# Kernel tuning notes

Hardware: AMD Instinct MI355X
Metric: run time of the kernel (lower is better)

## Reference

```python
import jax, jax.numpy as jnp
import numpy as np

R, S, C, HID = 8192, 128, 32, 64   # rays, samples/ray, grid_chn, mlp_hidden_chn
G = 128                            # voxel grid resolution
COLOR_CHN = 3
NUM_HARM = 3
OPACITY_INIT_BIAS = -5.0
GAIN = 1.0
HE_DIM = 3 * 2 * NUM_HARM + 3      # harmonic embedding dim = 21

def _relu(x):
    return jnp.maximum(x, 0.0)

def _trilinear(grid, p):
    # grid: [G, G, G, Cg] indexed [z, y, x]; p: [N, 3] xyz coords in [-1, 1]
    g = grid.shape[0]
    c = (p + 1.0) * 0.5 * (g - 1)  # align_corners=True convention
    c0f = jnp.floor(c)
    fr = c - c0f
    c0 = jnp.clip(c0f.astype(jnp.int32), 0, g - 1)
    c1 = jnp.clip(c0 + 1, 0, g - 1)
    x0, y0, z0 = c0[:, 0], c0[:, 1], c0[:, 2]
    x1, y1, z1 = c1[:, 0], c1[:, 1], c1[:, 2]
    fx, fy, fz = fr[:, 0:1], fr[:, 1:2], fr[:, 2:3]
    out = jnp.zeros((p.shape[0], grid.shape[-1]), grid.dtype)
    for xi, wx in ((x0, 1.0 - fx), (x1, fx)):
        for yi, wy in ((y0, 1.0 - fy), (y1, fy)):
            for zi, wz in ((z0, 1.0 - fz), (z1, fz)):
                out = out + (wx * wy * wz) * grid[zi, yi, xi]
    return out

def _harmonic(d):
    # [sin(2^i d), cos(2^i d)] for i<NUM_HARM, with raw direction appended
    freqs = 2.0 ** jnp.arange(NUM_HARM, dtype=jnp.float32)
    ang = d[:, None, :] * freqs[None, :, None]  # [R, NH, 3]
    n = d.shape[0]
    return jnp.concatenate([jnp.sin(ang).reshape(n, -1), jnp.cos(ang).reshape(n, -1), d], axis=-1)

def _forward(origins, directions, near, far, feature_grid, Wr, br, Wt1, bt1, Wt2, bt2, Wo1, bo1, Wo2, bo2, Wc1, bc1, Wc2, bc2):
    n_rays = origins.shape[0]
    # stratified midpoints between near and far
    t = near[:, None] + (far - near)[:, None] * (jnp.arange(S, dtype=jnp.float32) + 0.5) / S
    pts = origins[:, None, :] + t[..., None] * directions[:, None, :]  # [R, S, 3]
    feats = _trilinear(feature_grid, pts.reshape(-1, 3)).reshape(n_rays, S, -1)
    # trunk MLP
    e = _relu(feats @ Wt1 + bt1)
    e = _relu(e @ Wt2 + bt2)
    # opacity MLP (last-layer bias carries opacity_init_bias)
    raw = _relu(e @ Wo1 + bo1) @ Wo2 + bo2  # [R, S, 1]
    density = jax.nn.softplus(GAIN * raw[..., 0])
    delta = ((far - near) / S)[:, None]
    alpha = 1.0 - jnp.exp(-delta * density)  # [R, S]
    trans = jnp.cumprod(1.0 - alpha, axis=1)
    T = jnp.concatenate([jnp.ones((n_rays, 1), alpha.dtype), trans[:, :-1]], axis=1)
    w = T * alpha  # compositing weights
    # color branch: harmonic ray-direction encoding added to color-MLP input
    ray_enc = _harmonic(directions) @ Wr + br  # [R, HID]
    cin = e + ray_enc[:, None, :]
    col = jax.nn.sigmoid(_relu(cin @ Wc1 + bc1) @ Wc2 + bc2)  # [R, S, COLOR_CHN]
    color = jnp.einsum('rs,rsc->rc', w, col)
    mask = 1.0 - trans[:, -1]
    color = color + (1.0 - mask)[:, None] * 0.0  # bg_color = 0.0
    return color, mask

def setup_inputs():
    key = jax.random.key(0)
    ks = jax.random.split(key, 16)
    directions = jax.random.normal(ks[0], (R, 3), jnp.float32)
    directions = directions / jnp.linalg.norm(directions, axis=-1, keepdims=True)
    origins = jnp.zeros((R, 3), jnp.float32)
    near = jnp.full((R,), 0.1, jnp.float32)
    far = jnp.full((R,), 1.0, jnp.float32)
    feature_grid = jax.random.normal(ks[1], (G, G, G, C), jnp.float32) * 0.1
    def lin(k, i, o):
        s = (2.0 / (i + o)) ** 0.5
        return jax.random.normal(k, (i, o), jnp.float32) * s
    return {
        'origins': origins, 'directions': directions, 'near': near, 'far': far,
        'feature_grid': feature_grid,
        'Wr': lin(ks[2], HE_DIM, HID), 'br': jnp.zeros((HID,), jnp.float32),
        'Wt1': lin(ks[3], C, HID), 'bt1': jnp.zeros((HID,), jnp.float32),
        'Wt2': lin(ks[4], HID, HID), 'bt2': jnp.zeros((HID,), jnp.float32),
        'Wo1': lin(ks[5], HID, HID), 'bo1': jnp.zeros((HID,), jnp.float32),
        'Wo2': lin(ks[6], HID, 1), 'bo2': jnp.full((1,), OPACITY_INIT_BIAS, jnp.float32),
        'Wc1': lin(ks[7], HID, HID), 'bc1': jnp.zeros((HID,), jnp.float32),
        'Wc2': lin(ks[8], HID, COLOR_CHN), 'bc2': jnp.zeros((COLOR_CHN,), jnp.float32),
    }

def reference(origins, directions, near, far, feature_grid, Wr, br, Wt1, bt1, Wt2, bt2, Wo1, bo1, Wo2, bo2, Wc1, bc1, Wc2, bc2):
    return _forward(origins, directions, near, far, feature_grid, Wr, br, Wt1, bt1, Wt2, bt2, Wo1, bo1, Wo2, bo2, Wc1, bc1, Wc2, bc2)
```

## Files before the change

### kernel.cpp

```cpp
#include <hip/hip_runtime.h>
#include <hip/hip_bf16.h>
#include <math.h>

#define NRAYS 8192

typedef short s16x8 __attribute__((ext_vector_type(8)));
typedef float f32x4 __attribute__((ext_vector_type(4)));

__device__ __forceinline__ unsigned pk2(float a, float b){
  union { __hip_bfloat162 h; unsigned u; } cv;
  cv.h = __float22bfloat162_rn(make_float2(a, b));
  return cv.u;
}
__device__ __forceinline__ unsigned short f2bf(float x){
  unsigned u = __float_as_uint(x);
  u += 0x7FFF + ((u >> 16) & 1);
  return (unsigned short)(u >> 16);
}
__device__ __forceinline__ float softplusf_(float x){ return (x > 20.f) ? x : log1pf(expf(x)); }
__device__ __forceinline__ float sigmoidf_(float x){ return 1.f / (1.f + expf(-x)); }

__global__ void prep_weights(const float* __restrict__ Wt1, const float* __restrict__ Wt2,
                             const float* __restrict__ Wo1, const float* __restrict__ Wc1,
                             unsigned short* __restrict__ ws)
{
  const int i0 = blockIdx.x * blockDim.x + threadIdx.x;
  const int st = gridDim.x * blockDim.x;
  for (int i = i0; i < 2048; i += st){ int n = i >> 5, k = i & 31; ws[i]         = f2bf(Wt1[k * 64 + n]); }
  for (int i = i0; i < 4096; i += st){ int n = i >> 6, k = i & 63; ws[2048 + i]  = f2bf(Wt2[k * 64 + n]); }
  for (int i = i0; i < 4096; i += st){ int n = i >> 6, k = i & 63; ws[6144 + i]  = f2bf(Wo1[k * 64 + n]); }
  for (int i = i0; i < 4096; i += st){ int n = i >> 6, k = i & 63; ws[10240 + i] = f2bf(Wc1[k * 64 + n]); }
}

extern "C" __global__ __launch_bounds__(256, 4)
void lightplane_fwd(const float* __restrict__ origins, const float* __restrict__ dirs,
                    const float* __restrict__ nearv,   const float* __restrict__ farv,
                    const float* __restrict__ grid,
                    const float* __restrict__ Wr,  const float* __restrict__ br,
                    const float* __restrict__ bt1, const float* __restrict__ bt2,
                    const float* __restrict__ bo1,
                    const float* __restrict__ Wo2, const float* __restrict__ bo2,
                    const float* __restrict__ bc1,
                    const float* __restrict__ Wc2, const float* __restrict__ bc2,
                    const unsigned short* __restrict__ ws,
                    float* __restrict__ out)
{
  __shared__ float s_scr[4 * 2304];
  __shared__ float s_enc[2][64];
  __shared__ float s_wtot[2][2];
  __shared__ float s_part[2][2][3];

  const int tid  = threadIdx.x;
  const int lane = tid & 63, wv = tid >> 6;
  const int ln15 = lane & 15, quad = lane >> 4;
  const int r_loc = wv >> 1, hh = wv & 1;
  const int ray  = blockIdx.x * 2 + r_loc;
  const int s_idx = hh * 64 + lane;

  float*          wbase = s_scr + wv * 2304;
  unsigned*       uscr  = (unsigned*)wbase;
  unsigned short* fscr  = (unsigned short*)wbase;

  if (tid < 128) {
    const int rr = tid >> 6, j = tid & 63;
    const int rg = blockIdx.x * 2 + rr;
    const float ddx = dirs[rg * 3 + 0], ddy = dirs[rg * 3 + 1], ddz = dirs[rg * 3 + 2];
    float h[21]; float f = 1.f;
#pragma unroll
    for (int q = 0; q < 3; ++q) {
      h[q * 3 + 0] = sinf(ddx * f); h[q * 3 + 1] = sinf(ddy * f); h[q * 3 + 2] = sinf(ddz * f);
      h[9 + q * 3 + 0] = cosf(ddx * f); h[9 + q * 3 + 1] = cosf(ddy * f); h[9 + q * 3 + 2] = cosf(ddz * f);
      f *= 2.f;
    }
    h[18] = ddx; h[19] = ddy; h[20] = ddz;
    float a = br[j];
#pragma unroll
    for (int i = 0; i < 21; ++i) a = fmaf(h[i], Wr[i * 64 + j], a);
    s_enc[rr][j] = a;
  }

  const float dx = dirs[ray * 3 + 0], dy = dirs[ray * 3 + 1], dz = dirs[ray * 3 + 2];
  const float ox = origins[ray * 3 + 0], oy = origins[ray * 3 + 1], oz = origins[ray * 3 + 2];
  const float nr = nearv[ray], fa = farv[ray];
  const float t  = nr + (fa - nr) * ((s_idx + 0.5f) * (1.0f / 128.0f));
  const float px = fmaf(t, dx, ox), py = fmaf(t, dy, oy), pz = fmaf(t, dz, oz);

  const float cx = (px + 1.f) * 63.5f, cy = (py + 1.f) * 63.5f, cz = (pz + 1.f) * 63.5f;
  const float fx0 = floorf(cx), fy0 = floorf(cy), fz0 = floorf(cz);
  const float frx = cx - fx0, fry = cy - fy0, frz = cz - fz0;
  int ix0 = min(max((int)fx0, 0), 127), iy0 = min(max((int)fy0, 0), 127), iz0 = min(max((int)fz0, 0), 127);
  int ix1 = min(ix0 + 1, 127), iy1 = min(iy0 + 1, 127), iz1 = min(iz0 + 1, 127);
  const float wxs[2] = {1.f - frx, frx}, wys[2] = {1.f - fry, fry}, wzs[2] = {1.f - frz, frz};
  const int xi[2] = {ix0, ix1}, yi[2] = {iy0, iy1}, zi[2] = {iz0, iz1};

  float fe[32];
#pragma unroll
  for (int k = 0; k < 32; ++k) fe[k] = 0.f;
#pragma unroll
  for (int a = 0; a < 2; ++a)
#pragma unroll
    for (int b2i = 0; b2i < 2; ++b2i)
#pragma unroll
      for (int c2 = 0; c2 < 2; ++c2) {
        const float wgt = wzs[a] * wys[b2i] * wxs[c2];
        const float4* g4 = (const float4*)(grid + ((size_t)((zi[a] * 128 + yi[b2i]) * 128 + xi[c2])) * 32);
#pragma unroll
        for (int k = 0; k < 8; ++k) {
          float4 g = g4[k];
          fe[4 * k + 0] = fmaf(wgt, g.x, fe[4 * k + 0]);
          fe[4 * k + 1] = fmaf(wgt, g.y, fe[4 * k + 1]);
          fe[4 * k + 2] = fmaf(wgt, g.z, fe[4 * k + 2]);
          fe[4 * k + 3] = fmaf(wgt, g.w, fe[4 * k + 3]);
        }
      }

  {
    unsigned* frow = uscr + lane * 20;
#pragma unroll
    for (int q = 0; q < 4; ++q) {
      uint4 v;
      v.x = pk2(fe[8 * q + 0], fe[8 * q + 1]); v.y = pk2(fe[8 * q + 2], fe[8 * q + 3]);
      v.z = pk2(fe[8 * q + 4], fe[8 * q + 5]); v.w = pk2(fe[8 * q + 6], fe[8 * q + 7]);
      *(uint4*)(frow + 4 * q) = v;
    }
  }
  __syncthreads();

  s16x8 b1[4];
#pragma unroll
  for (int nt = 0; nt < 4; ++nt)
    b1[nt] = *(const s16x8*)(fscr + (16 * nt + ln15) * 40 + quad * 8);

#pragma unroll
  for (int mt = 0; mt < 4; ++mt) {
    s16x8 a1 = *(const s16x8*)(ws + (16 * mt + ln15) * 32 + quad * 8);
    float4 bb = *(const float4*)(bt1 + 16 * mt + 4 * quad);
    f32x4 acc[4];
#pragma unroll
    for (int nt = 0; nt < 4; ++nt) {
      f32x4 c; c[0] = bb.x; c[1] = bb.y; c[2] = bb.z; c[3] = bb.w;
      acc[nt] = __builtin_amdgcn_mfma_f32_16x16x32_bf16(a1, b1[nt], c, 0, 0, 0);
    }
#pragma unroll
    for (int nt = 0; nt < 4; ++nt) {
      uint2 p;
      p.x = pk2(fmaxf(acc[nt][0], 0.f), fmaxf(acc[nt][1], 0.f));
      p.y = pk2(fmaxf(acc[nt][2], 0.f), fmaxf(acc[nt][3], 0.f));
      *(uint2*)(uscr + (16 * nt + ln15) * 36 + 8 * mt + 2 * quad) = p;
    }
  }
  s16x8 b2[4][2];
#pragma unroll
  for (int nt = 0; nt < 4; ++nt)
#pragma unroll
    for (int ks = 0; ks < 2; ++ks)
      b2[nt][ks] = *(const s16x8*)(uscr + (16 * nt + ln15) * 36 + 16 * ks + 4 * quad);

#pragma unroll
  for (int mt = 0; mt < 4; ++mt) {
    float4 bb = *(const float4*)(bt2 + 16 * mt + 4 * quad);
    f32x4 acc[4];
#pragma unroll
    for (int nt = 0; nt < 4; ++nt) { f32x4 c; c[0]=bb.x;c[1]=bb.y;c[2]=bb.z;c[3]=bb.w; acc[nt]=c; }
#pragma unroll
    for (int ks = 0; ks < 2; ++ks) {
      s16x8 a = *(const s16x8*)(ws + 2048 + (16 * mt + ln15) * 64 + ks * 32 + quad * 8);
#pragma unroll
      for (int nt = 0; nt < 4; ++nt)
        acc[nt] = __builtin_amdgcn_mfma_f32_16x16x32_bf16(a, b2[nt][ks], acc[nt], 0, 0, 0);
    }
    float4 en = *(const float4*)(&s_enc[r_loc][16 * mt + 4 * quad]);
#pragma unroll
    for (int nt = 0; nt < 4; ++nt) {
      uint2 p;
      p.x = pk2(fmaxf(acc[nt][0], 0.f) + en.x, fmaxf(acc[nt][1], 0.f) + en.y);
      p.y = pk2(fmaxf(acc[nt][2], 0.f) + en.z, fmaxf(acc[nt][3], 0.f) + en.w);
      *(uint2*)(uscr + (16 * nt + ln15) * 36 + 8 * mt + 2 * quad) = p;
    }
  }
  s16x8 b4[4][2];
#pragma unroll
  for (int nt = 0; nt < 4; ++nt)
#pragma unroll
    for (int ks = 0; ks < 2; ++ks)
      b4[nt][ks] = *(const s16x8*)(uscr + (16 * nt + ln15) * 36 + 16 * ks + 4 * quad);

#pragma unroll
  for (int mt = 0; mt < 4; ++mt) {
    float4 bb = *(const float4*)(bt2 + 16 * mt + 4 * quad);
    f32x4 acc[4];
#pragma unroll
    for (int nt = 0; nt < 4; ++nt) { f32x4 c; c[0]=bb.x;c[1]=bb.y;c[2]=bb.z;c[3]=bb.w; acc[nt]=c; }
#pragma unroll
    for (int ks = 0; ks < 2; ++ks) {
      s16x8 a = *(const s16x8*)(ws + 2048 + (16 * mt + ln15) * 64 + ks * 32 + quad * 8);
#pragma unroll
      for (int nt = 0; nt < 4; ++nt)
        acc[nt] = __builtin_amdgcn_mfma_f32_16x16x32_bf16(a, b2[nt][ks], acc[nt], 0, 0, 0);
    }
#pragma unroll
    for (int nt = 0; nt < 4; ++nt) {
      uint2 p;
      p.x = pk2(fmaxf(acc[nt][0], 0.f), fmaxf(acc[nt][1], 0.f));
      p.y = pk2(fmaxf(acc[nt][2], 0.f), fmaxf(acc[nt][3], 0.f));
      *(uint2*)(uscr + (16 * nt + ln15) * 36 + 8 * mt + 2 * quad) = p;
    }
  }
  s16x8 b3[4][2];
#pragma unroll
  for (int nt = 0; nt < 4; ++nt)
#pragma unroll
    for (int ks = 0; ks < 2; ++ks)
      b3[nt][ks] = *(const s16x8*)(uscr + (16 * nt + ln15) * 36 + 16 * ks + 4 * quad);

  float p_o[4] = {0.f, 0.f, 0.f, 0.f};
  float pc0[4] = {0.f, 0.f, 0.f, 0.f}, pc1[4] = {0.f, 0.f, 0.f, 0.f}, pc2[4] = {0.f, 0.f, 0.f, 0.f};
#pragma unroll
  for (int mt = 0; mt < 4; ++mt) {
    {
      float4 bb = *(const float4*)(bo1 + 16 * mt + 4 * quad);
      f32x4 acc[4];
#pragma unroll
      for (int nt = 0; nt < 4; ++nt) { f32x4 c; c[0]=bb.x;c[1]=bb.y;c[2]=bb.z;c[3]=bb.w; acc[nt]=c; }
#pragma unroll
      for (int ks = 0; ks < 2; ++ks) {
        s16x8 a = *(const s16x8*)(ws + 6144 + (16 * mt + ln15) * 64 + ks * 32 + quad * 8);
#pragma unroll
        for (int nt = 0; nt < 4; ++nt)
          acc[nt] = __builtin_amdgcn_mfma_f32_16x16x32_bf16(a, b3[nt][ks], acc[nt], 0, 0, 0);
      }
      float4 wo = *(const float4*)(Wo2 + 16 * mt + 4 * quad);
#pragma unroll
      for (int nt = 0; nt < 4; ++nt)
        p_o[nt] += fmaxf(acc[nt][0], 0.f) * wo.x + fmaxf(acc[nt][1], 0.f) * wo.y +
                   fmaxf(acc[nt][2], 0.f) * wo.z + fmaxf(acc[nt][3], 0.f) * wo.w;
    }
    {
      float4 bb = *(const float4*)(bc1 + 16 * mt + 4 * quad);
      f32x4 acc[4];
#pragma unroll
      for (int nt = 0; nt < 4; ++nt) { f32x4 c; c[0]=bb.x;c[1]=bb.y;c[2]=bb.z;c[3]=bb.w; acc[nt]=c; }
#pragma unroll
      for (int ks = 0; ks < 2; ++ks) {
        s16x8 a = *(const s16x8*)(ws + 10240 + (16 * mt + ln15) * 64 + ks * 32 + quad * 8);
#pragma unroll
        for (int nt = 0; nt < 4; ++nt)
          acc[nt] = __builtin_amdgcn_mfma_f32_16x16x32_bf16(a, b4[nt][ks], acc[nt], 0, 0, 0);
      }
      float wcf[12];
      const float* wc = Wc2 + (16 * mt + 4 * quad) * 3;
      *(float4*)&wcf[0] = ((const float4*)wc)[0];
      *(float4*)&wcf[4] = ((const float4*)wc)[1];
      *(float4*)&wcf[8] = ((const float4*)wc)[2];
#pragma unroll
      for (int nt = 0; nt < 4; ++nt)
#pragma unroll
        for (int r = 0; r < 4; ++r) {
          const float hv = fmaxf(acc[nt][r], 0.f);
          pc0[nt] = fmaf(hv, wcf[r * 3 + 0], pc0[nt]);
          pc1[nt] = fmaf(hv, wcf[r * 3 + 1], pc1[nt]);
          pc2[nt] = fmaf(hv, wcf[r * 3 + 2], pc2[nt]);
        }
    }
  }
#pragma unroll
  for (int nt = 0; nt < 4; ++nt) {
    p_o[nt] += __shfl_xor(p_o[nt], 16, 64); p_o[nt] += __shfl_xor(p_o[nt], 32, 64);
    pc0[nt] += __shfl_xor(pc0[nt], 16, 64); pc0[nt] += __shfl_xor(pc0[nt], 32, 64);
    pc1[nt] += __shfl_xor(pc1[nt], 16, 64); pc1[nt] += __shfl_xor(pc1[nt], 32, 64);
    pc2[nt] += __shfl_xor(pc2[nt], 16, 64); pc2[nt] += __shfl_xor(pc2[nt], 32, 64);
  }

  const float delta = (fa - nr) * (1.0f / 128.0f);
  const float bo2v = bo2[0], bc2x = bc2[0], bc2y = bc2[1], bc2z = bc2[2];
  float A_[4], C0[4], C1[4], C2[4];
#pragma unroll
  for (int nt = 0; nt < 4; ++nt) {
    const float dens = softplusf_(p_o[nt] + bo2v);
    A_[nt] = 1.f - expf(-delta * dens);
    C0[nt] = sigmoidf_(pc0[nt] + bc2x);
    C1[nt] = sigmoidf_(pc1[nt] + bc2y);
    C2[nt] = sigmoidf_(pc2[nt] + bc2z);
  }
  const float a_own = (quad < 2) ? (quad == 0 ? A_[0] : A_[1]) : (quad == 2 ? A_[2] : A_[3]);
  const float c0own = (quad < 2) ? (quad == 0 ? C0[0] : C0[1]) : (quad == 2 ? C0[2] : C0[3]);
  const float c1own = (quad < 2) ? (quad == 0 ? C1[0] : C1[1]) : (quad == 2 ? C1[2] : C1[3]);
  const float c2own = (quad < 2) ? (quad == 0 ? C2[0] : C2[1]) : (quad == 2 ? C2[2] : C2[3]);

  float v = 1.f - a_own;
#pragma unroll
  for (int off = 1; off < 64; off <<= 1) {
    const float u = __shfl_up(v, off, 64);
    if (lane >= off) v *= u;
  }
  const float tot = __shfl(v, 63, 64);
  if (lane == 0) s_wtot[r_loc][hh] = tot;
  float excl = __shfl_up(v, 1, 64);
  if (lane == 0) excl = 1.f;
  __syncthreads();
  const float prefix = hh ? s_wtot[r_loc][0] : 1.f;
  const float Ttot   = s_wtot[r_loc][0] * s_wtot[r_loc][1];
  const float wgt = prefix * excl * a_own;

  float p0 = wgt * c0own, p1 = wgt * c1own, p2 = wgt * c2own;
#pragma unroll
  for (int off = 32; off > 0; off >>= 1) {
    p0 += __shfl_down(p0, off, 64);
    p1 += __shfl_down(p1, off, 64);
    p2 += __shfl_down(p2, off, 64);
  }
  if (lane == 0) { s_part[r_loc][hh][0] = p0; s_part[r_loc][hh][1] = p1; s_part[r_loc][hh][2] = p2; }
  __syncthreads();
  if (hh == 0 && lane == 0) {
    out[ray * 3 + 0] = s_part[r_loc][0][0] + s_part[r_loc][1][0];
    out[ray * 3 + 1] = s_part[r_loc][0][1] + s_part[r_loc][1][1];
    out[ray * 3 + 2] = s_part[r_loc][0][2] + s_part[r_loc][1][2];
    out[NRAYS * 3 + ray] = 1.f - Ttot;
  }
}

extern "C" void kernel_launch(void* const* d_in, const int* in_sizes, int n_in,
                              void* d_out, int out_size, void* d_ws, size_t ws_size,
                              hipStream_t stream)
{
  (void)in_sizes; (void)n_in; (void)out_size; (void)ws_size;
  const float* origins = (const float*)d_in[0];
  const float* dirs    = (const float*)d_in[1];
  const float* nearv   = (const float*)d_in[2];
  const float* farv    = (const float*)d_in[3];
  const float* grid    = (const float*)d_in[4];
  const float* Wr  = (const float*)d_in[5];
  const float* br  = (const float*)d_in[6];
  const float* Wt1 = (const float*)d_in[7];
  const float* bt1 = (const float*)d_in[8];
  const float* Wt2 = (const float*)d_in[9];
  const float* bt2 = (const float*)d_in[10];
  const float* Wo1 = (const float*)d_in[11];
  const float* bo1 = (const float*)d_in[12];
  const float* Wo2 = (const float*)d_in[13];
  const float* bo2 = (const float*)d_in[14];
  const float* Wc1 = (const float*)d_in[15];
  const float* bc1 = (const float*)d_in[16];
  const float* Wc2 = (const float*)d_in[17];
  const float* bc2 = (const float*)d_in[18];
  unsigned short* ws = (unsigned short*)d_ws;
  float* out = (float*)d_out;

  prep_weights<<<16, 256, 0, stream>>>(Wt1, Wt2, Wo1, Wc1, ws);
  lightplane_fwd<<<NRAYS / 2, 256, 0, stream>>>(origins, dirs, nearv, farv, grid,
                                                Wr, br, bt1, bt2, bo1, Wo2, bo2,
                                                bc1, Wc2, bc2, ws, out);
}
```

Measured before the change: 591.4 us.

## Compute trunk layer-2 GEMM once and add ray encoding in registers

The old code ran the second trunk GEMM twice: once with the ray encoding added for the color branch and once without it for the opacity branch. Now it runs once and feeds the result to the opacity MLP. It then adds the per-ray encoding to the bf16 B fragments in registers before the color GEMM, removing one GEMM and one LDS round trip. The extra bf16 rounding (bf16 value plus encoding, rounded again) differs slightly from rounding the fp32 sum. The launch-bounds occupancy hint is also lowered from 4 to 3 blocks per CU.

```diff
diff --git a/kernel.cpp b/kernel.cpp
--- a/kernel.cpp
+++ b/kernel.cpp
@@ -17,6 +17,7 @@
   u += 0x7FFF + ((u >> 16) & 1);
   return (unsigned short)(u >> 16);
 }
+__device__ __forceinline__ float bf2f(unsigned short s){ return __uint_as_float(((unsigned)s) << 16); }
 __device__ __forceinline__ float softplusf_(float x){ return (x > 20.f) ? x : log1pf(expf(x)); }
 __device__ __forceinline__ float sigmoidf_(float x){ return 1.f / (1.f + expf(-x)); }
 
@@ -32,7 +33,7 @@
   for (int i = i0; i < 4096; i += st){ int n = i >> 6, k = i & 63; ws[10240 + i] = f2bf(Wc1[k * 64 + n]); }
 }
 
-extern "C" __global__ __launch_bounds__(256, 4)
+extern "C" __global__ __launch_bounds__(256, 3)
 void lightplane_fwd(const float* __restrict__ origins, const float* __restrict__ dirs,
                     const float* __restrict__ nearv,   const float* __restrict__ farv,
                     const float* __restrict__ grid,
@@ -169,35 +170,6 @@
       for (int nt = 0; nt < 4; ++nt)
         acc[nt] = __builtin_amdgcn_mfma_f32_16x16x32_bf16(a, b2[nt][ks], acc[nt], 0, 0, 0);
     }
-    float4 en = *(const float4*)(&s_enc[r_loc][16 * mt + 4 * quad]);
-#pragma unroll
-    for (int nt = 0; nt < 4; ++nt) {
-      uint2 p;
-      p.x = pk2(fmaxf(acc[nt][0], 0.f) + en.x, fmaxf(acc[nt][1], 0.f) + en.y);
-      p.y = pk2(fmaxf(acc[nt][2], 0.f) + en.z, fmaxf(acc[nt][3], 0.f) + en.w);
-      *(uint2*)(uscr + (16 * nt + ln15) * 36 + 8 * mt + 2 * quad) = p;
-    }
-  }
-  s16x8 b4[4][2];
-#pragma unroll
-  for (int nt = 0; nt < 4; ++nt)
-#pragma unroll
-    for (int ks = 0; ks < 2; ++ks)
-      b4[nt][ks] = *(const s16x8*)(uscr + (16 * nt + ln15) * 36 + 16 * ks + 4 * quad);
-
-#pragma unroll
-  for (int mt = 0; mt < 4; ++mt) {
-    float4 bb = *(const float4*)(bt2 + 16 * mt + 4 * quad);
-    f32x4 acc[4];
-#pragma unroll
-    for (int nt = 0; nt < 4; ++nt) { f32x4 c; c[0]=bb.x;c[1]=bb.y;c[2]=bb.z;c[3]=bb.w; acc[nt]=c; }
-#pragma unroll
-    for (int ks = 0; ks < 2; ++ks) {
-      s16x8 a = *(const s16x8*)(ws + 2048 + (16 * mt + ln15) * 64 + ks * 32 + quad * 8);
-#pragma unroll
-      for (int nt = 0; nt < 4; ++nt)
-        acc[nt] = __builtin_amdgcn_mfma_f32_16x16x32_bf16(a, b2[nt][ks], acc[nt], 0, 0, 0);
-    }
 #pragma unroll
     for (int nt = 0; nt < 4; ++nt) {
       uint2 p;
@@ -214,55 +186,73 @@
       b3[nt][ks] = *(const s16x8*)(uscr + (16 * nt + ln15) * 36 + 16 * ks + 4 * quad);
 
   float p_o[4] = {0.f, 0.f, 0.f, 0.f};
+#pragma unroll
+  for (int mt = 0; mt < 4; ++mt) {
+    float4 bb = *(const float4*)(bo1 + 16 * mt + 4 * quad);
+    f32x4 acc[4];
+#pragma unroll
+    for (int nt = 0; nt < 4; ++nt) { f32x4 c; c[0]=bb.x;c[1]=bb.y;c[2]=bb.z;c[3]=bb.w; acc[nt]=c; }
+#pragma unroll
+    for (int ks = 0; ks < 2; ++ks) {
+      s16x8 a = *(const s16x8*)(ws + 6144 + (16 * mt + ln15) * 64 + ks * 32 + quad * 8);
+#pragma unroll
+      for (int nt = 0; nt < 4; ++nt)
+        acc[nt] = __builtin_amdgcn_mfma_f32_16x16x32_bf16(a, b3[nt][ks], acc[nt], 0, 0, 0);
+    }
+    float4 wo = *(const float4*)(Wo2 + 16 * mt + 4 * quad);
+#pragma unroll
+    for (int nt = 0; nt < 4; ++nt)
+      p_o[nt] += fmaxf(acc[nt][0], 0.f) * wo.x + fmaxf(acc[nt][1], 0.f) * wo.y +
+                 fmaxf(acc[nt][2], 0.f) * wo.z + fmaxf(acc[nt][3], 0.f) * wo.w;
+  }
+
+#pragma unroll
+  for (int ks = 0; ks < 2; ++ks) {
+    const float* ep = &s_enc[r_loc][ks * 32 + quad * 8];
+    float4 e0 = *(const float4*)ep;
+    float4 e1 = *(const float4*)(ep + 4);
+    const float encv[8] = {e0.x, e0.y, e0.z, e0.w, e1.x, e1.y, e1.z, e1.w};
+#pragma unroll
+    for (int nt = 0; nt < 4; ++nt) {
+      s16x8 v = b3[nt][ks];
+      s16x8 r;
+#pragma unroll
+      for (int j = 0; j < 8; ++j)
+        r[j] = (short)f2bf(bf2f((unsigned short)v[j]) + encv[j]);
+      b3[nt][ks] = r;
+    }
+  }
+
   float pc0[4] = {0.f, 0.f, 0.f, 0.f}, pc1[4] = {0.f, 0.f, 0.f, 0.f}, pc2[4] = {0.f, 0.f, 0.f, 0.f};
 #pragma unroll
   for (int mt = 0; mt < 4; ++mt) {
-    {
-      float4 bb = *(const float4*)(bo1 + 16 * mt + 4 * quad);
-      f32x4 acc[4];
-#pragma unroll
-      for (int nt = 0; nt < 4; ++nt) { f32x4 c; c[0]=bb.x;c[1]=bb.y;c[2]=bb.z;c[3]=bb.w; acc[nt]=c; }
-#pragma unroll
-      for (int ks = 0; ks < 2; ++ks) {
-        s16x8 a = *(const s16x8*)(ws + 6144 + (16 * mt + ln15) * 64 + ks * 32 + quad * 8);
-#pragma unroll
-        for (int nt = 0; nt < 4; ++nt)
-          acc[nt] = __builtin_amdgcn_mfma_f32_16x16x32_bf16(a, b3[nt][ks], acc[nt], 0, 0, 0);
+    float4 bb = *(const float4*)(bc1 + 16 * mt + 4 * quad);
+    f32x4 acc[4];
+#pragma unroll
+    for (int nt = 0; nt < 4; ++nt) { f32x4 c; c[0]=bb.x;c[1]=bb.y;c[2]=bb.z;c[3]=bb.w; acc[nt]=c; }
+#pragma unroll
+    for (int ks = 0; ks < 2; ++ks) {
+      s16x8 a = *(const s16x8*)(ws + 10240 + (16 * mt + ln15) * 64 + ks * 32 + quad * 8);
+#pragma unroll
+      for (int nt = 0; nt < 4; ++nt)
+        acc[nt] = __builtin_amdgcn_mfma_f32_16x16x32_bf16(a, b3[nt][ks], acc[nt], 0, 0, 0);
+    }
+    float wcf[12];
+    const float* wc = Wc2 + (16 * mt + 4 * quad) * 3;
+    *(float4*)&wcf[0] = ((const float4*)wc)[0];
+    *(float4*)&wcf[4] = ((const float4*)wc)[1];
+    *(float4*)&wcf[8] = ((const float4*)wc)[2];
+#pragma unroll
+    for (int nt = 0; nt < 4; ++nt)
+#pragma unroll
+      for (int r = 0; r < 4; ++r) {
+        const float hv = fmaxf(acc[nt][r], 0.f);
+        pc0[nt] = fmaf(hv, wcf[r * 3 + 0], pc0[nt]);
+        pc1[nt] = fmaf(hv, wcf[r * 3 + 1], pc1[nt]);
+        pc2[nt] = fmaf(hv, wcf[r * 3 + 2], pc2[nt]);
       }
-      float4 wo = *(const float4*)(Wo2 + 16 * mt + 4 * quad);
-#pragma unroll
-      for (int nt = 0; nt < 4; ++nt)
-        p_o[nt] += fmaxf(acc[nt][0], 0.f) * wo.x + fmaxf(acc[nt][1], 0.f) * wo.y +
-                   fmaxf(acc[nt][2], 0.f) * wo.z + fmaxf(acc[nt][3], 0.f) * wo.w;
-    }
-    {
-      float4 bb = *(const float4*)(bc1 + 16 * mt + 4 * quad);
-      f32x4 acc[4];
-#pragma unroll
-      for (int nt = 0; nt < 4; ++nt) { f32x4 c; c[0]=bb.x;c[1]=bb.y;c[2]=bb.z;c[3]=bb.w; acc[nt]=c; }
-#pragma unroll
-      for (int ks = 0; ks < 2; ++ks) {
-        s16x8 a = *(const s16x8*)(ws + 10240 + (16 * mt + ln15) * 64 + ks * 32 + quad * 8);
-#pragma unroll
-        for (int nt = 0; nt < 4; ++nt)
-          acc[nt] = __builtin_amdgcn_mfma_f32_16x16x32_bf16(a, b4[nt][ks], acc[nt], 0, 0, 0);
-      }
-      float wcf[12];
-      const float* wc = Wc2 + (16 * mt + 4 * quad) * 3;
-      *(float4*)&wcf[0] = ((const float4*)wc)[0];
-      *(float4*)&wcf[4] = ((const float4*)wc)[1];
-      *(float4*)&wcf[8] = ((const float4*)wc)[2];
-#pragma unroll
-      for (int nt = 0; nt < 4; ++nt)
-#pragma unroll
-        for (int r = 0; r < 4; ++r) {
-          const float hv = fmaxf(acc[nt][r], 0.f);
-          pc0[nt] = fmaf(hv, wcf[r * 3 + 0], pc0[nt]);
-          pc1[nt] = fmaf(hv, wcf[r * 3 + 1], pc1[nt]);
-          pc2[nt] = fmaf(hv, wcf[r * 3 + 2], pc2[nt]);
-        }
-    }
-  }
+  }
+
 #pragma unroll
   for (int nt = 0; nt < 4; ++nt) {
     p_o[nt] += __shfl_xor(p_o[nt], 16, 64); p_o[nt] += __shfl_xor(p_o[nt], 32, 64);
```

Measured after the change: 511.5 us. 13.5% less time.
